# Kernel tuning notes

Measured on AMD Instinct MI355X. Metric: run time of the kernel, lower is better.

## Reference

```python
import jax, jax.numpy as jnp
import numpy as np

N_NODES, N_EDGES = 50000, 800000
IN_X, OUT_X = 32, 64
IN_EN, OUT_EN = 32, 64
HIDDEN = [64, 128, 32]  # build_mlp hidden sizes


def _mlp_params(key, dims):
    ps = []
    for i, (a, b) in enumerate(zip(dims[:-1], dims[1:])):
        k1, k2, key = jax.random.split(key, 3)
        s = 1.0 / np.sqrt(a)
        ps.append(jax.random.uniform(k1, (a, b), jnp.float32, -s, s))
        ps.append(jax.random.uniform(k2, (b,), jnp.float32, -s, s))
    return ps


def _mlp_apply(h, params):
    n_layers = len(params) // 2
    for i in range(n_layers):
        W, b = params[2 * i], params[2 * i + 1]
        h = h @ W + b
        if i < n_layers - 1:
            h = jax.nn.relu(h)
    return h


def setup_inputs() -> dict:
    key = jax.random.key(0)
    kx, ken, ks, kd, kt, kp, k_ten, k_pen = jax.random.split(key, 8)
    inp = {
        "x": jax.random.normal(kx, (N_NODES, IN_X), jnp.float32),
        "en": jax.random.normal(ken, (N_NODES, IN_EN), jnp.float32),
        "src": jax.random.randint(ks, (N_EDGES,), 0, N_NODES),
        "dst": jax.random.randint(kd, (N_EDGES,), 0, N_NODES),
    }
    # linear layers theta/phi for x
    kt1, kt2 = jax.random.split(kt)
    kp1, kp2 = jax.random.split(kp)
    s = 1.0 / np.sqrt(IN_X)
    inp["theta_W"] = jax.random.uniform(kt1, (IN_X, OUT_X), jnp.float32, -s, s)
    inp["theta_b"] = jax.random.uniform(kt2, (OUT_X,), jnp.float32, -s, s)
    inp["phi_W"] = jax.random.uniform(kp1, (IN_X, OUT_X), jnp.float32, -s, s)
    inp["phi_b"] = jax.random.uniform(kp2, (OUT_X,), jnp.float32, -s, s)
    # MLPs theta_en / phi_en: in_en -> 64 -> 128 -> 32 -> out_en
    dims = [IN_EN] + HIDDEN + [OUT_EN]
    for name, p in zip(
        ["ten_W0", "ten_b0", "ten_W1", "ten_b1", "ten_W2", "ten_b2", "ten_W3", "ten_b3"],
        _mlp_params(k_ten, dims)):
        inp[name] = p
    for name, p in zip(
        ["pen_W0", "pen_b0", "pen_W1", "pen_b1", "pen_W2", "pen_b2", "pen_W3", "pen_b3"],
        _mlp_params(k_pen, dims)):
        inp[name] = p
    return inp


def reference(x, en, src, dst,
              theta_W, theta_b, phi_W, phi_b,
              ten_W0, ten_b0, ten_W1, ten_b1, ten_W2, ten_b2, ten_W3, ten_b3,
              pen_W0, pen_b0, pen_W1, pen_b1, pen_W2, pen_b2, pen_W3, pen_b3):
    n = x.shape[0]
    ten = [ten_W0, ten_b0, ten_W1, ten_b1, ten_W2, ten_b2, ten_W3, ten_b3]
    pen = [pen_W0, pen_b0, pen_W1, pen_b1, pen_W2, pen_b2, pen_W3, pen_b3]

    # --- message: per-edge features ---
    dx = x[dst] - x[src]                       # [E, in_x]
    edge_x = dx @ theta_W + theta_b + (x @ phi_W + phi_b)[src]   # [E, out_x]
    den = en[dst] - en[src]                    # [E, in_en]
    edge_en = _mlp_apply(den, ten) + _mlp_apply(en, pen)[src]    # [E, out_en]

    # --- aggregate: max over incoming edge_x, mean over incoming edge_en ---
    deg = jax.ops.segment_sum(jnp.ones((src.shape[0],), x.dtype), dst, num_segments=n)
    has_in = (deg > 0)[:, None]
    x_new = jax.ops.segment_max(edge_x, dst, num_segments=n)
    x_new = jnp.where(has_in, x_new, 0.0)      # DGL zero-fills empty nodes
    en_sum = jax.ops.segment_sum(edge_en, dst, num_segments=n)
    en_new = en_sum / jnp.maximum(deg, 1.0)[:, None]

    # knn_graph rebuild is a library call (excluded from the kernel target);
    # return the updated node features carried by the new graph.
    return jnp.concatenate([x_new, en_new], axis=-1)  # [N, out_x + out_en]
```

## Files before the change

### kernel.cpp

```cpp
#include <hip/hip_runtime.h>

#define N_NODES 50000
#define N_EDGES 800000

typedef __attribute__((ext_vector_type(8))) short short8v;
typedef __attribute__((ext_vector_type(4))) float f32x4;

__device__ __forceinline__ ushort bf16hi(float v) {
  return (ushort)(__float_as_uint(v) >> 16);
}

__device__ __forceinline__ void split8(const float v[8], short8v& hh, short8v& ll) {
#pragma unroll
  for (int j = 0; j < 8; ++j) {
    unsigned uv = __float_as_uint(v[j]);
    hh[j] = (short)(uv >> 16);
    float hf = __uint_as_float(uv & 0xFFFF0000u);
    ll[j] = (short)(__float_as_uint(v[j] - hf) >> 16);
  }
}

#define C1_X 196
#define C1_CNT 3125
#define C1_PACK 120

constexpr int XK_THT = 0;
constexpr int XK_PHT = 2048;
constexpr int XK_THB = 4096;
constexpr int XK_PHB = 4160;
constexpr int XK_SZ  = 4224;

__global__ void __launch_bounds__(256) combo1_kernel(
    const float* __restrict__ x,
    const float* __restrict__ thW, const float* __restrict__ thB,
    const float* __restrict__ phW, const float* __restrict__ phB,
    float* __restrict__ out, float* __restrict__ gp,
    const int* __restrict__ dst, int* __restrict__ counts,
    const float* __restrict__ tW1, const float* __restrict__ tW2,
    const float* __restrict__ tW0, const float* __restrict__ pW0,
    const float* __restrict__ pW1, const float* __restrict__ pW2,
    const float* __restrict__ pW3, ushort* __restrict__ wp) {
  const int b = blockIdx.x;
  const int tid = threadIdx.x;
  if (b < C1_X) {
    __shared__ __align__(16) float sm[XK_SZ];
    for (int t = tid; t < 2048; t += 256) {
      int j = t >> 5, k = t & 31;
      sm[XK_THT + t] = thW[k * 64 + j];
      sm[XK_PHT + t] = phW[k * 64 + j];
    }
    for (int t = tid; t < 64; t += 256) {
      sm[XK_THB + t] = thB[t];
      sm[XK_PHB + t] = phB[t];
    }
    __syncthreads();
    int n = b * 256 + tid;
    if (n >= N_NODES) return;

    float xv[32];
    {
      const float4* p = (const float4*)(x + (long)n * 32);
#pragma unroll
      for (int q = 0; q < 8; ++q) {
        float4 v = p[q];
        xv[q * 4 + 0] = v.x; xv[q * 4 + 1] = v.y;
        xv[q * 4 + 2] = v.z; xv[q * 4 + 3] = v.w;
      }
    }
    float* ao = out + (long)n * 128;
    float* go = gp + (long)n * 128;
    for (int j = 0; j < 64; ++j) {
      float dth = 0.f, dph = 0.f;
#pragma unroll
      for (int k = 0; k < 32; ++k) {
        dth += xv[k] * sm[XK_THT + j * 32 + k];
        dph += xv[k] * sm[XK_PHT + j * 32 + k];
      }
      ao[j] = sm[XK_THB + j] + dth;
      go[j] = sm[XK_PHB + j] + dph - dth;
    }
  } else if (b < C1_X + C1_CNT) {
    int e = (b - C1_X) * 256 + tid;
    if (e < N_EDGES) atomicAdd(&counts[dst[e]], 1);
  } else {
    int t = (b - C1_X - C1_CNT) * 256 + tid;
    if (t >= 30720) return;
    float v;
    int hi_off, lo_off;
    if (t < 8192) {
      int fi = t >> 9, lane = (t >> 3) & 63, j = t & 7;
      int r = fi >> 1, f = fi & 1;
      int k2 = r * 16 + (lane & 15);
      int jg = f * 32 + (lane >> 4) * 8 + j;
      v = tW1[jg * 128 + k2];
      hi_off = t; lo_off = 8192 + t;
    } else if (t < 12288) {
      int t2 = t - 8192;
      int fi = t2 >> 9, lane = (t2 >> 3) & 63, j = t2 & 7;
      int tt = fi >> 2, f2 = fi & 3;
      int cc = tt * 16 + (lane & 15);
      int qq = (lane >> 4) & 3;
      int k2 = f2 * 32 + (j >> 2) * 16 + qq * 4 + (j & 3);
      v = tW2[k2 * 32 + cc];
      hi_off = 16384 + t2; lo_off = 20480 + t2;
    } else if (t < 16384) {
      int t3 = t - 12288;
      const float* M = (t3 < 2048) ? tW0 : pW0;
      int tt3 = t3 & 2047;
      int fi = tt3 >> 9, lane = (tt3 >> 3) & 63, j = tt3 & 7;
      int row = fi * 16 + (lane & 15);
      int k = (lane >> 4) * 8 + j;
      v = M[k * 64 + row];
      hi_off = ((t3 < 2048) ? 24576 : 28672) + tt3;
      lo_off = hi_off + 2048;
    } else if (t < 24576) {
      int t5 = t - 16384;
      int fi = t5 >> 9, lane = (t5 >> 3) & 63, j = t5 & 7;
      int r = fi >> 1, f = fi & 1;
      int row = r * 16 + (lane & 15);
      int sig = 32 * f + 16 * (j >> 2) + 4 * ((lane >> 4) & 3) + (j & 3);
      v = pW1[sig * 128 + row];
      hi_off = 32768 + t5; lo_off = 40960 + t5;
    } else if (t < 28672) {
      int t6 = t - 24576;
      int fi = t6 >> 9, lane = (t6 >> 3) & 63, j = t6 & 7;
      int tt = fi >> 2, f2 = fi & 3;
      int cc = tt * 16 + (lane & 15);
      int qq = (lane >> 4) & 3;
      int k2 = f2 * 32 + (j >> 2) * 16 + qq * 4 + (j & 3);
      v = pW2[k2 * 32 + cc];
      hi_off = 49152 + t6; lo_off = 53248 + t6;
    } else {
      int t7 = t - 28672;
      int fi = t7 >> 9, lane = (t7 >> 3) & 63, j = t7 & 7;
      int row = fi * 16 + (lane & 15);
      int sig = 16 * (j >> 2) + 4 * ((lane >> 4) & 3) + (j & 3);
      v = pW3[sig * 64 + row];
      hi_off = 57344 + t7; lo_off = 59392 + t7;
    }
    ushort h = bf16hi(v);
    float hf = __uint_as_float((unsigned)h << 16);
    ushort l = bf16hi(v - hf);
    wp[hi_off] = h;
    wp[lo_off] = l;
  }
}

#define SCAN_NB ((N_NODES + 1023) / 1024)

__global__ void __launch_bounds__(1024) scan1_kernel(
    const int* __restrict__ counts, int* __restrict__ offsets,
    int* __restrict__ bsum) {
  __shared__ int wsum[16];
  int t = threadIdx.x, b = blockIdx.x;
  int idx = b * 1024 + t;
  int c = (idx < N_NODES) ? counts[idx] : 0;
  int lane = t & 63, w = t >> 6;
  int v = c;
#pragma unroll
  for (int off = 1; off < 64; off <<= 1) {
    int tt = __shfl_up(v, off);
    if (lane >= off) v += tt;
  }
  if (lane == 63) wsum[w] = v;
  __syncthreads();
  int wpre = 0;
#pragma unroll
  for (int i = 0; i < 16; ++i) {
    int tt = wsum[i];
    if (i < w) wpre += tt;
  }
  int incl = v + wpre;
  if (idx < N_NODES) offsets[idx] = incl - c;
  if (t == 1023) bsum[b] = incl;
}

__global__ void __launch_bounds__(1024) scan2_kernel(
    const int* __restrict__ bsum, int* __restrict__ offsets,
    int* __restrict__ counts) {
  __shared__ int sb[SCAN_NB];
  int t = threadIdx.x, b = blockIdx.x;
  if (t < SCAN_NB) sb[t] = bsum[t];
  __syncthreads();
  int bpre = 0;
#pragma unroll
  for (int i = 0; i < SCAN_NB; ++i) {
    int tt = sb[i];
    if (i < b) bpre += tt;
  }
  int idx = b * 1024 + t;
  if (idx < N_NODES) {
    int v = offsets[idx] + bpre;
    offsets[idx] = v;
    counts[idx] = v;
  }
  if (b == 0 && t == 0) offsets[N_NODES] = N_EDGES;
}

#define C2_EN 391
#define C2_SC 1563

__global__ void __launch_bounds__(512) combo2_kernel(
    const float* __restrict__ en, const ushort* __restrict__ wp,
    const float* __restrict__ pb0, const float* __restrict__ pb1,
    const float* __restrict__ pb2, const float* __restrict__ pb3,
    float* __restrict__ u, float* __restrict__ gp,
    const int* __restrict__ src, const int* __restrict__ dst,
    int* __restrict__ cursor, int2* __restrict__ csr) {
  const int b = blockIdx.x;
  const int tid = threadIdx.x;
  if (b < C2_EN) {
    __shared__ __align__(16) ushort lds[36864];
    {
      const uint4* s4 = (const uint4*)(wp + 24576);
      uint4* d4 = (uint4*)lds;
      for (int i = tid; i < 4608; i += 512) d4[i] = s4[i];
    }
    __syncthreads();
    const int lane = tid & 63, q = lane >> 4, c = lane & 15, wv = tid >> 6;
    const int n = (b * 8 + wv) * 16 + c;
    const bool valid = n < N_NODES;

    float env[8];
#pragma unroll
    for (int j = 0; j < 8; ++j) env[j] = 0.f;
    if (valid) {
      const float4* p = (const float4*)(en + (long)n * 32 + q * 8);
      float4 e0 = p[0], e1 = p[1];
      env[0] = e0.x; env[1] = e0.y; env[2] = e0.z; env[3] = e0.w;
      env[4] = e1.x; env[5] = e1.y; env[6] = e1.z; env[7] = e1.w;
    }
    short8v beh, bel;
    split8(env, beh, bel);

    const short8v* TW0H = (const short8v*)(lds);
    const short8v* TW0L = (const short8v*)(lds + 2048);
    const short8v* PW0H = (const short8v*)(lds + 4096);
    const short8v* PW0L = (const short8v*)(lds + 6144);
    const short8v* NW1H = (const short8v*)(lds + 8192);
    const short8v* NW1L = (const short8v*)(lds + 16384);
    const short8v* NW2H = (const short8v*)(lds + 24576);
    const short8v* NW2L = (const short8v*)(lds + 28672);
    const short8v* NW3H = (const short8v*)(lds + 32768);
    const short8v* NW3L = (const short8v*)(lds + 34816);

#pragma unroll
    for (int t = 0; t < 4; ++t) {
      f32x4 a = {0.f, 0.f, 0.f, 0.f};
      short8v ah = TW0H[t * 64 + lane], al = TW0L[t * 64 + lane];
      a = __builtin_amdgcn_mfma_f32_16x16x32_bf16(ah, beh, a, 0, 0, 0);
      a = __builtin_amdgcn_mfma_f32_16x16x32_bf16(al, beh, a, 0, 0, 0);
      a = __builtin_amdgcn_mfma_f32_16x16x32_bf16(ah, bel, a, 0, 0, 0);
      if (valid) *(f32x4*)(u + (long)n * 64 + t * 16 + q * 4) = a;
    }

    float h0v[4][4];
#pragma unroll
    for (int t = 0; t < 4; ++t) {
      f32x4 a = *(const f32x4*)(pb0 + t * 16 + q * 4);
      short8v ah = PW0H[t * 64 + lane], al = PW0L[t * 64 + lane];
      a = __builtin_amdgcn_mfma_f32_16x16x32_bf16(ah, beh, a, 0, 0, 0);
      a = __builtin_amdgcn_mfma_f32_16x16x32_bf16(al, beh, a, 0, 0, 0);
      a = __builtin_amdgcn_mfma_f32_16x16x32_bf16(ah, bel, a, 0, 0, 0);
#pragma unroll
      for (int g = 0; g < 4; ++g) h0v[t][g] = fmaxf(a[g], 0.f);
    }

    short8v b1h[2], b1l[2];
#pragma unroll
    for (int f = 0; f < 2; ++f) {
      float tmp[8];
#pragma unroll
      for (int j = 0; j < 8; ++j) tmp[j] = h0v[2 * f + (j >> 2)][j & 3];
      split8(tmp, b1h[f], b1l[f]);
    }

    float h1v[8][4];
#pragma unroll
    for (int r = 0; r < 8; ++r) {
      f32x4 a = *(const f32x4*)(pb1 + r * 16 + q * 4);
#pragma unroll
      for (int f = 0; f < 2; ++f) {
        short8v ah = NW1H[(r * 2 + f) * 64 + lane];
        short8v al = NW1L[(r * 2 + f) * 64 + lane];
        a = __builtin_amdgcn_mfma_f32_16x16x32_bf16(ah, b1h[f], a, 0, 0, 0);
        a = __builtin_amdgcn_mfma_f32_16x16x32_bf16(al, b1h[f], a, 0, 0, 0);
        a = __builtin_amdgcn_mfma_f32_16x16x32_bf16(ah, b1l[f], a, 0, 0, 0);
      }
#pragma unroll
      for (int g = 0; g < 4; ++g) h1v[r][g] = fmaxf(a[g], 0.f);
    }

    short8v b2h[4], b2l[4];
#pragma unroll
    for (int f2 = 0; f2 < 4; ++f2) {
      float tmp[8];
#pragma unroll
      for (int j = 0; j < 8; ++j) tmp[j] = h1v[2 * f2 + (j >> 2)][j & 3];
      split8(tmp, b2h[f2], b2l[f2]);
    }

    float h2v[2][4];
#pragma unroll
    for (int tt = 0; tt < 2; ++tt) {
      f32x4 a = *(const f32x4*)(pb2 + tt * 16 + q * 4);
#pragma unroll
      for (int f2 = 0; f2 < 4; ++f2) {
        short8v ah = NW2H[(tt * 4 + f2) * 64 + lane];
        short8v al = NW2L[(tt * 4 + f2) * 64 + lane];
        a = __builtin_amdgcn_mfma_f32_16x16x32_bf16(ah, b2h[f2], a, 0, 0, 0);
        a = __builtin_amdgcn_mfma_f32_16x16x32_bf16(al, b2h[f2], a, 0, 0, 0);
        a = __builtin_amdgcn_mfma_f32_16x16x32_bf16(ah, b2l[f2], a, 0, 0, 0);
      }
#pragma unroll
      for (int g = 0; g < 4; ++g) h2v[tt][g] = fmaxf(a[g], 0.f);
    }

    short8v b3h, b3l;
    {
      float tmp[8];
#pragma unroll
      for (int j = 0; j < 8; ++j) tmp[j] = h2v[j >> 2][j & 3];
      split8(tmp, b3h, b3l);
    }

#pragma unroll
    for (int t = 0; t < 4; ++t) {
      f32x4 a = *(const f32x4*)(pb3 + t * 16 + q * 4);
      short8v ah = NW3H[t * 64 + lane], al = NW3L[t * 64 + lane];
      a = __builtin_amdgcn_mfma_f32_16x16x32_bf16(ah, b3h, a, 0, 0, 0);
      a = __builtin_amdgcn_mfma_f32_16x16x32_bf16(al, b3h, a, 0, 0, 0);
      a = __builtin_amdgcn_mfma_f32_16x16x32_bf16(ah, b3l, a, 0, 0, 0);
      if (valid) *(f32x4*)(gp + (long)n * 128 + 64 + t * 16 + q * 4) = a;
    }
  } else {
    int e = (b - C2_EN) * 512 + tid;
    if (e >= N_EDGES) return;
    int d = dst[e];
    int slot = atomicAdd(&cursor[d], 1);
    csr[slot] = make_int2(src[e], d);
  }
}

__global__ void __launch_bounds__(1024) mlp_edge_kernel(
    const float* __restrict__ u,
    const int2* __restrict__ csr,
    const float* __restrict__ b0g, const float* __restrict__ b1g,
    const float* __restrict__ b2g,
    const ushort* __restrict__ wp,
    float* __restrict__ h2sum) {
  __shared__ __align__(16) ushort lds[24576];
  {
    const uint4* s4 = (const uint4*)wp;
    uint4* d4 = (uint4*)lds;
    for (int i = threadIdx.x; i < 3072; i += 1024) d4[i] = s4[i];
  }
  __syncthreads();

  const int orig = blockIdx.x;
  const int xcd = orig & 7, loc = orig >> 3;
  const int blk = (xcd < 5) ? xcd * 391 + loc
                            : 5 * 391 + (xcd - 5) * 390 + loc;

  const int lane = threadIdx.x & 63;
  const int q = lane >> 4, c = lane & 15;
  const int wv = threadIdx.x >> 6;
  const int e = (blk * 16 + wv) * 16 + c;
  const int2 pr = csr[e];
  const int s = pr.x, d = pr.y;

  const short8v* W1HI = (const short8v*)(lds);
  const short8v* W1LO = (const short8v*)(lds + 8192);
  const short8v* W2HI = (const short8v*)(lds + 16384);
  const short8v* W2LO = (const short8v*)(lds + 20480);

  short8v bh0, bl0, bh1, bl1;
  {
    const float* ud = u + (long)d * 64 + q * 8;
    const float* us = u + (long)s * 64 + q * 8;
    const float* bp = b0g + q * 8;
#pragma unroll
    for (int f = 0; f < 2; ++f) {
      float4 d0 = *(const float4*)(ud + f * 32);
      float4 d1 = *(const float4*)(ud + f * 32 + 4);
      float4 s0 = *(const float4*)(us + f * 32);
      float4 s1 = *(const float4*)(us + f * 32 + 4);
      float4 c0 = *(const float4*)(bp + f * 32);
      float4 c1 = *(const float4*)(bp + f * 32 + 4);
      float v[8];
      v[0] = fmaxf(d0.x - s0.x + c0.x, 0.f);
      v[1] = fmaxf(d0.y - s0.y + c0.y, 0.f);
      v[2] = fmaxf(d0.z - s0.z + c0.z, 0.f);
      v[3] = fmaxf(d0.w - s0.w + c0.w, 0.f);
      v[4] = fmaxf(d1.x - s1.x + c1.x, 0.f);
      v[5] = fmaxf(d1.y - s1.y + c1.y, 0.f);
      v[6] = fmaxf(d1.z - s1.z + c1.z, 0.f);
      v[7] = fmaxf(d1.w - s1.w + c1.w, 0.f);
      short8v hh, ll;
      split8(v, hh, ll);
      if (f == 0) { bh0 = hh; bl0 = ll; } else { bh1 = hh; bl1 = ll; }
    }
  }

  f32x4 acc[8];
#pragma unroll
  for (int r = 0; r < 8; ++r)
    acc[r] = *(const f32x4*)(b1g + r * 16 + q * 4);
#pragma unroll
  for (int r = 0; r < 8; ++r) {
    short8v ah0 = W1HI[(2 * r) * 64 + lane];
    short8v ah1 = W1HI[(2 * r + 1) * 64 + lane];
    short8v al0 = W1LO[(2 * r) * 64 + lane];
    short8v al1 = W1LO[(2 * r + 1) * 64 + lane];
    acc[r] = __builtin_amdgcn_mfma_f32_16x16x32_bf16(ah0, bh0, acc[r], 0, 0, 0);
    acc[r] = __builtin_amdgcn_mfma_f32_16x16x32_bf16(ah1, bh1, acc[r], 0, 0, 0);
    acc[r] = __builtin_amdgcn_mfma_f32_16x16x32_bf16(al0, bh0, acc[r], 0, 0, 0);
    acc[r] = __builtin_amdgcn_mfma_f32_16x16x32_bf16(al1, bh1, acc[r], 0, 0, 0);
    acc[r] = __builtin_amdgcn_mfma_f32_16x16x32_bf16(ah0, bl0, acc[r], 0, 0, 0);
    acc[r] = __builtin_amdgcn_mfma_f32_16x16x32_bf16(ah1, bl1, acc[r], 0, 0, 0);
  }
  float h1v[8][4];
#pragma unroll
  for (int r = 0; r < 8; ++r)
#pragma unroll
    for (int g = 0; g < 4; ++g) h1v[r][g] = fmaxf(acc[r][g], 0.f);

  short8v b2h[4], b2l[4];
#pragma unroll
  for (int f2 = 0; f2 < 4; ++f2) {
    float tmp[8];
#pragma unroll
    for (int j = 0; j < 8; ++j) tmp[j] = h1v[2 * f2 + (j >> 2)][j & 3];
    split8(tmp, b2h[f2], b2l[f2]);
  }

  f32x4 a20 = *(const f32x4*)(b2g + q * 4);
  f32x4 a21 = *(const f32x4*)(b2g + 16 + q * 4);
#pragma unroll
  for (int f2 = 0; f2 < 4; ++f2) {
    short8v ah = W2HI[f2 * 64 + lane];
    short8v al = W2LO[f2 * 64 + lane];
    a20 = __builtin_amdgcn_mfma_f32_16x16x32_bf16(ah, b2h[f2], a20, 0, 0, 0);
    a20 = __builtin_amdgcn_mfma_f32_16x16x32_bf16(al, b2h[f2], a20, 0, 0, 0);
    a20 = __builtin_amdgcn_mfma_f32_16x16x32_bf16(ah, b2l[f2], a20, 0, 0, 0);
    short8v ah1 = W2HI[(4 + f2) * 64 + lane];
    short8v al1 = W2LO[(4 + f2) * 64 + lane];
    a21 = __builtin_amdgcn_mfma_f32_16x16x32_bf16(ah1, b2h[f2], a21, 0, 0, 0);
    a21 = __builtin_amdgcn_mfma_f32_16x16x32_bf16(al1, b2h[f2], a21, 0, 0, 0);
    a21 = __builtin_amdgcn_mfma_f32_16x16x32_bf16(ah1, b2l[f2], a21, 0, 0, 0);
  }
  float h2v[8];
#pragma unroll
  for (int g = 0; g < 4; ++g) {
    h2v[g] = fmaxf(a20[g], 0.f);
    h2v[4 + g] = fmaxf(a21[g], 0.f);
  }

  int dp = __shfl_up(d, 1, 16);
  bool head = (c == 0) || (dp != d);
  int seg = head ? c : 0;
#pragma unroll
  for (int off = 1; off < 16; off <<= 1) {
    int t = __shfl_up(seg, off, 16);
    if (c >= off) seg = max(seg, t);
  }
#pragma unroll
  for (int off = 1; off < 16; off <<= 1) {
    bool take = (c - off) >= seg;
#pragma unroll
    for (int k = 0; k < 8; ++k) {
      float t = __shfl_up(h2v[k], off, 16);
      if (take) h2v[k] += t;
    }
  }
  int dn = __shfl_down(d, 1, 16);
  bool tail = (c == 15) || (dn != d);
  if (tail) {
    float* hs = h2sum + (long)d * 32 + q * 4;
#pragma unroll
    for (int g = 0; g < 4; ++g) atomicAdd(&hs[g], h2v[g]);
#pragma unroll
    for (int g = 0; g < 4; ++g) atomicAdd(&hs[16 + g], h2v[4 + g]);
  }
}

__global__ void __launch_bounds__(256) gather_kernel(
    const int2* __restrict__ csr, const int* __restrict__ offsets,
    const float* __restrict__ gp, const float* __restrict__ h2sum,
    const float* __restrict__ tW3, const float* __restrict__ tb3,
    float* __restrict__ out) {
  __shared__ float sW3[2048 + 64];
  for (int t = threadIdx.x; t < 2048; t += 256) sW3[t] = tW3[t];
  for (int t = threadIdx.x; t < 64; t += 256) sW3[2048 + t] = tb3[t];
  __syncthreads();
  int n = blockIdx.x * 8 + (threadIdx.x >> 5);
  int l = threadIdx.x & 31;
  int half = l >> 4, j4 = l & 15;
  int off = half * 64 + j4 * 4;
  int o0 = offsets[n], o1 = offsets[n + 1];
  int deg = o1 - o0;

  const float NEG = -3.402823466e38f;
  float4 mx = make_float4(NEG, NEG, NEG, NEG);
  float4 sm4 = make_float4(0.f, 0.f, 0.f, 0.f);
  for (int t = o0; t < o1; ++t) {
    int s = csr[t].x;
    float4 v = *(const float4*)(gp + (long)s * 128 + off);
    mx.x = fmaxf(mx.x, v.x); mx.y = fmaxf(mx.y, v.y);
    mx.z = fmaxf(mx.z, v.z); mx.w = fmaxf(mx.w, v.w);
    sm4.x += v.x; sm4.y += v.y; sm4.z += v.z; sm4.w += v.w;
  }

  float4 r;
  if (half == 0) {
    float4 a = *(const float4*)(out + (long)n * 128 + off);
    bool has = deg > 0;
    r.x = has ? a.x + mx.x : 0.f;
    r.y = has ? a.y + mx.y : 0.f;
    r.z = has ? a.z + mx.z : 0.f;
    r.w = has ? a.w + mx.w : 0.f;
  } else {
    int jj = j4 * 4;
    float w30 = 0.f, w31 = 0.f, w32 = 0.f, w33 = 0.f;
    const float* h2r = h2sum + (long)n * 32;
#pragma unroll
    for (int k = 0; k < 32; ++k) {
      float h = h2r[k];
      const float* wrow = &sW3[k * 64 + jj];
      w30 += h * wrow[0]; w31 += h * wrow[1];
      w32 += h * wrow[2]; w33 += h * wrow[3];
    }
    float dg = (float)deg;
    float inv = 1.f / fmaxf(dg, 1.f);
    r.x = (sm4.x + w30 + dg * sW3[2048 + jj + 0]) * inv;
    r.y = (sm4.y + w31 + dg * sW3[2048 + jj + 1]) * inv;
    r.z = (sm4.z + w32 + dg * sW3[2048 + jj + 2]) * inv;
    r.w = (sm4.w + w33 + dg * sW3[2048 + jj + 3]) * inv;
  }
  *(float4*)(out + (long)n * 128 + off) = r;
}

extern "C" void kernel_launch(void* const* d_in, const int* in_sizes, int n_in,
                              void* d_out, int out_size, void* d_ws,
                              size_t ws_size, hipStream_t stream) {
  const float* x   = (const float*)d_in[0];
  const float* en  = (const float*)d_in[1];
  const int* src   = (const int*)d_in[2];
  const int* dst   = (const int*)d_in[3];
  const float* thW = (const float*)d_in[4];
  const float* thB = (const float*)d_in[5];
  const float* phW = (const float*)d_in[6];
  const float* phB = (const float*)d_in[7];
  const float* tW0 = (const float*)d_in[8];
  const float* tb0 = (const float*)d_in[9];
  const float* tW1 = (const float*)d_in[10];
  const float* tb1 = (const float*)d_in[11];
  const float* tW2 = (const float*)d_in[12];
  const float* tb2 = (const float*)d_in[13];
  const float* tW3 = (const float*)d_in[14];
  const float* tb3 = (const float*)d_in[15];
  const float* pW0 = (const float*)d_in[16];
  const float* pb0 = (const float*)d_in[17];
  const float* pW1 = (const float*)d_in[18];
  const float* pb1 = (const float*)d_in[19];
  const float* pW2 = (const float*)d_in[20];
  const float* pb2 = (const float*)d_in[21];
  const float* pW3 = (const float*)d_in[22];
  const float* pb3 = (const float*)d_in[23];

  float* out = (float*)d_out;
  float* ws  = (float*)d_ws;
  float* gp     = ws;
  float* u      = ws + (long)N_NODES * 128;
  float* h2sum  = ws + (long)N_NODES * 192;
  float* wpf    = ws + (long)N_NODES * 224;
  ushort* wp    = (ushort*)wpf;
  int* iw       = (int*)(wpf + 30720);
  int2* csr     = (int2*)iw;
  int* counts   = iw + 2 * N_EDGES;
  int* offsets  = counts + N_NODES;
  int* bsum     = offsets + N_NODES + 1;

  hipMemsetAsync(counts, 0, N_NODES * sizeof(int), stream);
  hipMemsetAsync(h2sum, 0, (size_t)N_NODES * 32 * sizeof(float), stream);
  combo1_kernel<<<C1_X + C1_CNT + C1_PACK, 256, 0, stream>>>(
      x, thW, thB, phW, phB, out, gp, dst, counts,
      tW1, tW2, tW0, pW0, pW1, pW2, pW3, wp);
  scan1_kernel<<<SCAN_NB, 1024, 0, stream>>>(counts, offsets, bsum);
  scan2_kernel<<<SCAN_NB, 1024, 0, stream>>>(bsum, offsets, counts);
  combo2_kernel<<<C2_EN + C2_SC, 512, 0, stream>>>(
      en, wp, pb0, pb1, pb2, pb3, u, gp, src, dst, counts, csr);
  mlp_edge_kernel<<<3125, 1024, 0, stream>>>(
      u, csr, tb0, tb1, tb2, wp, h2sum);
  gather_kernel<<<N_NODES / 8, 256, 0, stream>>>(
      csr, offsets, gp, h2sum, tW3, tb3, out);
}
```

Measured before the change: 325.6 us.

## Compute first theta_en layer per edge from en difference instead of precomputed u

Removes the per-node precompute of en@tW0 (u buffer) and instead gathers en[dst]-en[src] (32 floats) per edge and runs the first MLP layer with MFMA inside the edge kernel. Gathered bytes per edge are halved (32 vs 64 floats per endpoint) and the u write/read pass disappears. The cost is three extra MFMAs per tile per edge, more LDS for W0, and a reordering of the W1 packing to match the new input layout.

Result: faster. 315.2 us (median of 2 runs) (-3.2%).

```diff
diff --git a/kernel.cpp b/kernel.cpp
--- a/kernel.cpp
+++ b/kernel.cpp
@@ -90,9 +90,9 @@
     if (t < 8192) {
       int fi = t >> 9, lane = (t >> 3) & 63, j = t & 7;
       int r = fi >> 1, f = fi & 1;
-      int k2 = r * 16 + (lane & 15);
-      int jg = f * 32 + (lane >> 4) * 8 + j;
-      v = tW1[jg * 128 + k2];
+      int row = r * 16 + (lane & 15);
+      int sig = 32 * f + 16 * (j >> 2) + 4 * ((lane >> 4) & 3) + (j & 3);
+      v = tW1[sig * 128 + row];
       hi_off = t; lo_off = 8192 + t;
     } else if (t < 12288) {
       int t2 = t - 8192;
@@ -103,16 +103,20 @@
       int k2 = f2 * 32 + (j >> 2) * 16 + qq * 4 + (j & 3);
       v = tW2[k2 * 32 + cc];
       hi_off = 16384 + t2; lo_off = 20480 + t2;
-    } else if (t < 16384) {
+    } else if (t < 14336) {
       int t3 = t - 12288;
-      const float* M = (t3 < 2048) ? tW0 : pW0;
-      int tt3 = t3 & 2047;
-      int fi = tt3 >> 9, lane = (tt3 >> 3) & 63, j = tt3 & 7;
+      int fi = t3 >> 9, lane = (t3 >> 3) & 63, j = t3 & 7;
       int row = fi * 16 + (lane & 15);
       int k = (lane >> 4) * 8 + j;
-      v = M[k * 64 + row];
-      hi_off = ((t3 < 2048) ? 24576 : 28672) + tt3;
-      lo_off = hi_off + 2048;
+      v = tW0[k * 64 + row];
+      hi_off = 24576 + t3; lo_off = 26624 + t3;
+    } else if (t < 16384) {
+      int t4 = t - 14336;
+      int fi = t4 >> 9, lane = (t4 >> 3) & 63, j = t4 & 7;
+      int row = fi * 16 + (lane & 15);
+      int k = (lane >> 4) * 8 + j;
+      v = pW0[k * 64 + row];
+      hi_off = 28672 + t4; lo_off = 30720 + t4;
     } else if (t < 24576) {
       int t5 = t - 16384;
       int fi = t5 >> 9, lane = (t5 >> 3) & 63, j = t5 & 7;
@@ -204,17 +208,17 @@
     const float* __restrict__ en, const ushort* __restrict__ wp,
     const float* __restrict__ pb0, const float* __restrict__ pb1,
     const float* __restrict__ pb2, const float* __restrict__ pb3,
-    float* __restrict__ u, float* __restrict__ gp,
+    float* __restrict__ gp,
     const int* __restrict__ src, const int* __restrict__ dst,
     int* __restrict__ cursor, int2* __restrict__ csr) {
   const int b = blockIdx.x;
   const int tid = threadIdx.x;
   if (b < C2_EN) {
-    __shared__ __align__(16) ushort lds[36864];
+    __shared__ __align__(16) ushort lds[32768];
     {
-      const uint4* s4 = (const uint4*)(wp + 24576);
+      const uint4* s4 = (const uint4*)(wp + 28672);
       uint4* d4 = (uint4*)lds;
-      for (int i = tid; i < 4608; i += 512) d4[i] = s4[i];
+      for (int i = tid; i < 4096; i += 512) d4[i] = s4[i];
     }
     __syncthreads();
     const int lane = tid & 63, q = lane >> 4, c = lane & 15, wv = tid >> 6;
@@ -233,26 +237,14 @@
     short8v beh, bel;
     split8(env, beh, bel);
 
-    const short8v* TW0H = (const short8v*)(lds);
-    const short8v* TW0L = (const short8v*)(lds + 2048);
-    const short8v* PW0H = (const short8v*)(lds + 4096);
-    const short8v* PW0L = (const short8v*)(lds + 6144);
-    const short8v* NW1H = (const short8v*)(lds + 8192);
-    const short8v* NW1L = (const short8v*)(lds + 16384);
-    const short8v* NW2H = (const short8v*)(lds + 24576);
-    const short8v* NW2L = (const short8v*)(lds + 28672);
-    const short8v* NW3H = (const short8v*)(lds + 32768);
-    const short8v* NW3L = (const short8v*)(lds + 34816);
-
-#pragma unroll
-    for (int t = 0; t < 4; ++t) {
-      f32x4 a = {0.f, 0.f, 0.f, 0.f};
-      short8v ah = TW0H[t * 64 + lane], al = TW0L[t * 64 + lane];
-      a = __builtin_amdgcn_mfma_f32_16x16x32_bf16(ah, beh, a, 0, 0, 0);
-      a = __builtin_amdgcn_mfma_f32_16x16x32_bf16(al, beh, a, 0, 0, 0);
-      a = __builtin_amdgcn_mfma_f32_16x16x32_bf16(ah, bel, a, 0, 0, 0);
-      if (valid) *(f32x4*)(u + (long)n * 64 + t * 16 + q * 4) = a;
-    }
+    const short8v* PW0H = (const short8v*)(lds);
+    const short8v* PW0L = (const short8v*)(lds + 2048);
+    const short8v* NW1H = (const short8v*)(lds + 4096);
+    const short8v* NW1L = (const short8v*)(lds + 12288);
+    const short8v* NW2H = (const short8v*)(lds + 20480);
+    const short8v* NW2L = (const short8v*)(lds + 24576);
+    const short8v* NW3H = (const short8v*)(lds + 28672);
+    const short8v* NW3L = (const short8v*)(lds + 30720);
 
     float h0v[4][4];
 #pragma unroll
@@ -343,17 +335,17 @@
 }
 
 __global__ void __launch_bounds__(1024) mlp_edge_kernel(
-    const float* __restrict__ u,
+    const float* __restrict__ en,
     const int2* __restrict__ csr,
     const float* __restrict__ b0g, const float* __restrict__ b1g,
     const float* __restrict__ b2g,
     const ushort* __restrict__ wp,
     float* __restrict__ h2sum) {
-  __shared__ __align__(16) ushort lds[24576];
+  __shared__ __align__(16) ushort lds[28672];
   {
     const uint4* s4 = (const uint4*)wp;
     uint4* d4 = (uint4*)lds;
-    for (int i = threadIdx.x; i < 3072; i += 1024) d4[i] = s4[i];
+    for (int i = threadIdx.x; i < 3584; i += 1024) d4[i] = s4[i];
   }
   __syncthreads();
 
@@ -373,57 +365,58 @@
   const short8v* W1LO = (const short8v*)(lds + 8192);
   const short8v* W2HI = (const short8v*)(lds + 16384);
   const short8v* W2LO = (const short8v*)(lds + 20480);
-
-  short8v bh0, bl0, bh1, bl1;
+  const short8v* W0H  = (const short8v*)(lds + 24576);
+  const short8v* W0L  = (const short8v*)(lds + 26624);
+
+  short8v dh, dl;
   {
-    const float* ud = u + (long)d * 64 + q * 8;
-    const float* us = u + (long)s * 64 + q * 8;
-    const float* bp = b0g + q * 8;
+    const float4* pd = (const float4*)(en + (long)d * 32 + q * 8);
+    const float4* ps = (const float4*)(en + (long)s * 32 + q * 8);
+    float4 a0 = pd[0], a1 = pd[1], b0 = ps[0], b1 = ps[1];
+    float v[8];
+    v[0] = a0.x - b0.x; v[1] = a0.y - b0.y;
+    v[2] = a0.z - b0.z; v[3] = a0.w - b0.w;
+    v[4] = a1.x - b1.x; v[5] = a1.y - b1.y;
+    v[6] = a1.z - b1.z; v[7] = a1.w - b1.w;
+    split8(v, dh, dl);
+  }
+
+  float h0v[4][4];
+#pragma unroll
+  for (int t = 0; t < 4; ++t) {
+    f32x4 a = *(const f32x4*)(b0g + t * 16 + q * 4);
+    short8v ah = W0H[t * 64 + lane], al = W0L[t * 64 + lane];
+    a = __builtin_amdgcn_mfma_f32_16x16x32_bf16(ah, dh, a, 0, 0, 0);
+    a = __builtin_amdgcn_mfma_f32_16x16x32_bf16(al, dh, a, 0, 0, 0);
+    a = __builtin_amdgcn_mfma_f32_16x16x32_bf16(ah, dl, a, 0, 0, 0);
+#pragma unroll
+    for (int g = 0; g < 4; ++g) h0v[t][g] = fmaxf(a[g], 0.f);
+  }
+
+  short8v b1h[2], b1l[2];
+#pragma unroll
+  for (int f = 0; f < 2; ++f) {
+    float tmp[8];
+#pragma unroll
+    for (int j = 0; j < 8; ++j) tmp[j] = h0v[2 * f + (j >> 2)][j & 3];
+    split8(tmp, b1h[f], b1l[f]);
+  }
+
+  float h1v[8][4];
+#pragma unroll
+  for (int r = 0; r < 8; ++r) {
+    f32x4 a = *(const f32x4*)(b1g + r * 16 + q * 4);
 #pragma unroll
     for (int f = 0; f < 2; ++f) {
-      float4 d0 = *(const float4*)(ud + f * 32);
-      float4 d1 = *(const float4*)(ud + f * 32 + 4);
-      float4 s0 = *(const float4*)(us + f * 32);
-      float4 s1 = *(const float4*)(us + f * 32 + 4);
-      float4 c0 = *(const float4*)(bp + f * 32);
-      float4 c1 = *(const float4*)(bp + f * 32 + 4);
-      float v[8];
-      v[0] = fmaxf(d0.x - s0.x + c0.x, 0.f);
-      v[1] = fmaxf(d0.y - s0.y + c0.y, 0.f);
-      v[2] = fmaxf(d0.z - s0.z + c0.z, 0.f);
-      v[3] = fmaxf(d0.w - s0.w + c0.w, 0.f);
-      v[4] = fmaxf(d1.x - s1.x + c1.x, 0.f);
-      v[5] = fmaxf(d1.y - s1.y + c1.y, 0.f);
-      v[6] = fmaxf(d1.z - s1.z + c1.z, 0.f);
-      v[7] = fmaxf(d1.w - s1.w + c1.w, 0.f);
-      short8v hh, ll;
-      split8(v, hh, ll);
-      if (f == 0) { bh0 = hh; bl0 = ll; } else { bh1 = hh; bl1 = ll; }
-    }
-  }
-
-  f32x4 acc[8];
-#pragma unroll
-  for (int r = 0; r < 8; ++r)
-    acc[r] = *(const f32x4*)(b1g + r * 16 + q * 4);
-#pragma unroll
-  for (int r = 0; r < 8; ++r) {
-    short8v ah0 = W1HI[(2 * r) * 64 + lane];
-    short8v ah1 = W1HI[(2 * r + 1) * 64 + lane];
-    short8v al0 = W1LO[(2 * r) * 64 + lane];
-    short8v al1 = W1LO[(2 * r + 1) * 64 + lane];
-    acc[r] = __builtin_amdgcn_mfma_f32_16x16x32_bf16(ah0, bh0, acc[r], 0, 0, 0);
-    acc[r] = __builtin_amdgcn_mfma_f32_16x16x32_bf16(ah1, bh1, acc[r], 0, 0, 0);
-    acc[r] = __builtin_amdgcn_mfma_f32_16x16x32_bf16(al0, bh0, acc[r], 0, 0, 0);
-    acc[r] = __builtin_amdgcn_mfma_f32_16x16x32_bf16(al1, bh1, acc[r], 0, 0, 0);
-    acc[r] = __builtin_amdgcn_mfma_f32_16x16x32_bf16(ah0, bl0, acc[r], 0, 0, 0);
-    acc[r] = __builtin_amdgcn_mfma_f32_16x16x32_bf16(ah1, bl1, acc[r], 0, 0, 0);
-  }
-  float h1v[8][4];
-#pragma unroll
-  for (int r = 0; r < 8; ++r)
-#pragma unroll
-    for (int g = 0; g < 4; ++g) h1v[r][g] = fmaxf(acc[r][g], 0.f);
+      short8v ah = W1HI[(r * 2 + f) * 64 + lane];
+      short8v al = W1LO[(r * 2 + f) * 64 + lane];
+      a = __builtin_amdgcn_mfma_f32_16x16x32_bf16(ah, b1h[f], a, 0, 0, 0);
+      a = __builtin_amdgcn_mfma_f32_16x16x32_bf16(al, b1h[f], a, 0, 0, 0);
+      a = __builtin_amdgcn_mfma_f32_16x16x32_bf16(ah, b1l[f], a, 0, 0, 0);
+    }
+#pragma unroll
+    for (int g = 0; g < 4; ++g) h1v[r][g] = fmaxf(a[g], 0.f);
+  }
 
   short8v b2h[4], b2l[4];
 #pragma unroll
@@ -571,9 +564,8 @@
   float* out = (float*)d_out;
   float* ws  = (float*)d_ws;
   float* gp     = ws;
-  float* u      = ws + (long)N_NODES * 128;
-  float* h2sum  = ws + (long)N_NODES * 192;
-  float* wpf    = ws + (long)N_NODES * 224;
+  float* h2sum  = ws + (long)N_NODES * 128;
+  float* wpf    = ws + (long)N_NODES * 160;
   ushort* wp    = (ushort*)wpf;
   int* iw       = (int*)(wpf + 30720);
   int2* csr     = (int2*)iw;
@@ -589,9 +581,9 @@
   scan1_kernel<<<SCAN_NB, 1024, 0, stream>>>(counts, offsets, bsum);
   scan2_kernel<<<SCAN_NB, 1024, 0, stream>>>(bsum, offsets, counts);
   combo2_kernel<<<C2_EN + C2_SC, 512, 0, stream>>>(
-      en, wp, pb0, pb1, pb2, pb3, u, gp, src, dst, counts, csr);
+      en, wp, pb0, pb1, pb2, pb3, gp, src, dst, counts, csr);
   mlp_edge_kernel<<<3125, 1024, 0, stream>>>(
-      u, csr, tb0, tb1, tb2, wp, h2sum);
+      en, csr, tb0, tb1, tb2, wp, h2sum);
   gather_kernel<<<N_NODES / 8, 256, 0, stream>>>(
       csr, offsets, gp, h2sum, tW3, tb3, out);
 }
```
